# Kernel tuning notes

Hardware: AMD Instinct MI355X
Metric: run time of the kernel (lower is better)

## Reference

```python
import jax, jax.numpy as jnp
import numpy as np

HID = 5120
H_DEV = 16          # 128 heads / 8 devices
NOPE = 128
ROPE = 64
VDIM = 128
QH = NOPE + ROPE    # 192
Q_LORA = 1536
KV_LORA = 512
EPS = 1e-6
SCALE_DEV = 1.0 / 8.0
ROPE_BASE = 10000.0


def rmsnorm(x, w):
    var = jnp.mean(x * x, axis=-1, keepdims=True)
    return x * jax.lax.rsqrt(var + EPS) * w


def apply_rope(x, pos):
    # DeepSeek-V2: interleaved->blocked reorder, then rotate-half RoPE.
    d = x.shape[-1]
    x = jnp.concatenate([x[..., 0::2], x[..., 1::2]], axis=-1)
    inv = 1.0 / (ROPE_BASE ** (jnp.arange(0, d, 2, dtype=jnp.float32) / d))  # [d/2]
    ang = pos[:, None, :, None].astype(jnp.float32) * inv                     # [b,1,s,d/2]
    cos = jnp.concatenate([jnp.cos(ang), jnp.cos(ang)], axis=-1)
    sin = jnp.concatenate([jnp.sin(ang), jnp.sin(ang)], axis=-1)
    x1, x2 = x[..., : d // 2], x[..., d // 2:]
    return x * cos + jnp.concatenate([-x2, x1], axis=-1) * sin


def setup_inputs() -> dict:
    key = jax.random.key(0)
    ks = jax.random.split(key, 16)
    b, s, past = 1, 2048, 2048
    w = lambda k, shape: (jax.random.normal(k, shape, jnp.float32) * 0.02)
    return {
        "hidden_states": jax.random.normal(ks[0], (b, s, HID), jnp.float32),
        "position_ids": jnp.arange(b * s, dtype=jnp.int32).reshape(b, s),
        "attention_mask": jnp.zeros((b, 1, s, past + s), jnp.float32),
        "past_k": jax.random.normal(ks[1], (b, H_DEV, past, QH), jnp.float32),
        "past_v": jax.random.normal(ks[2], (b, H_DEV, past, VDIM), jnp.float32),
        "w_in_ln": jnp.ones((HID,), jnp.float32),
        "w_qa": w(ks[3], (Q_LORA, HID)),
        "w_qa_ln": jnp.ones((Q_LORA,), jnp.float32),
        "w_qb": w(ks[4], (H_DEV * QH, Q_LORA)),
        "w_kva": w(ks[5], (KV_LORA + ROPE, HID)),
        "w_kva_ln": jnp.ones((KV_LORA,), jnp.float32),
        "w_kvb": w(ks[6], (H_DEV * (NOPE + VDIM), KV_LORA)),
        "w_o": w(ks[7], (HID, H_DEV * VDIM)),
    }


def reference(hidden_states, position_ids, attention_mask, past_k, past_v,
              w_in_ln, w_qa, w_qa_ln, w_qb, w_kva, w_kva_ln, w_kvb, w_o):
    b, s, _ = hidden_states.shape
    residual = hidden_states * SCALE_DEV
    x = rmsnorm(hidden_states, w_in_ln)

    # MLA query: low-rank down, RMSNorm, up to per-device heads
    q = rmsnorm(x @ w_qa.T, w_qa_ln) @ w_qb.T                       # [b,s,H*QH]
    q = q.reshape(b, s, H_DEV, QH).transpose(0, 2, 1, 3)            # [b,H,s,QH]
    q_nope, q_pe = q[..., :NOPE], q[..., NOPE:]

    # MLA key/value: joint compressed kv + shared rope key
    ckv = x @ w_kva.T                                                # [b,s,KV_LORA+ROPE]
    c_kv, k_pe = ckv[..., :KV_LORA], ckv[..., KV_LORA:]
    kv = rmsnorm(c_kv, w_kva_ln) @ w_kvb.T                           # [b,s,H*(NOPE+V)]
    kv = kv.reshape(b, s, H_DEV, NOPE + VDIM).transpose(0, 2, 1, 3)  # [b,H,s,NOPE+V]
    k_nope, v = kv[..., :NOPE], kv[..., NOPE:]
    k_pe = k_pe.reshape(b, 1, s, ROPE)

    q_pe = apply_rope(q_pe, position_ids)
    k_pe = apply_rope(k_pe, position_ids)

    q = jnp.concatenate([q_nope, q_pe], axis=-1)                     # [b,H,s,QH]
    k = jnp.concatenate([k_nope, jnp.broadcast_to(k_pe, (b, H_DEV, s, ROPE))], axis=-1)

    # KV-cache concat -> present kv
    k = jnp.concatenate([past_k, k], axis=2)                         # [b,H,s_kv,QH]
    v = jnp.concatenate([past_v, v], axis=2)                         # [b,H,s_kv,V]

    scores = jnp.einsum('bhqd,bhkd->bhqk', q, k) * (QH ** -0.5) + attention_mask
    attn = jax.nn.softmax(scores, axis=-1)
    ctx = jnp.einsum('bhqk,bhkd->bhqd', attn, v)                     # [b,H,s,V]
    ctx = ctx.transpose(0, 2, 1, 3).reshape(b, s, H_DEV * VDIM)

    out = residual + ctx @ w_o.T
    return out.astype(jnp.float32), k.astype(jnp.float32), v.astype(jnp.float32)
```

## Files before the change

### kernel.cpp

```cpp
#include <hip/hip_runtime.h>
#include <cstdint>

typedef unsigned short ushort_t;
typedef __attribute__((ext_vector_type(8))) short short8;
typedef __attribute__((ext_vector_type(4))) float floatx4;

#define HID    5120
#define NHEAD  16
#define NOPE   128
#define ROPE_D 64
#define VDIM   128
#define QHD    192
#define QLORA  1536
#define KVLORA 512
#define SEQ    2048
#define PAST   2048
#define TOTK   4096
#define EPS_RMS 1e-6f
#define SCALE_DEV 0.125f
#define LOG2E 1.4426950408889634f
#define ATT_SCALE 0.07216878364870322f
#define LOG2_10000 13.287712379549449f

__device__ __forceinline__ float bf2f(ushort_t u) {
  unsigned int x = ((unsigned int)u) << 16;
  return __builtin_bit_cast(float, x);
}
__device__ __forceinline__ ushort_t f2bf(float f) {
  unsigned int u = __builtin_bit_cast(unsigned int, f);
  unsigned int r = u + 0x7fffu + ((u >> 16) & 1u);
  return (ushort_t)(r >> 16);
}
__device__ __forceinline__ void unpack8(uint4 c, float* f) {
  const ushort_t* p = (const ushort_t*)&c;
#pragma unroll
  for (int i = 0; i < 8; ++i) f[i] = bf2f(p[i]);
}
__device__ __forceinline__ uint4 pack8(const float* f) {
  uint4 c;
  ushort_t* p = (ushort_t*)&c;
#pragma unroll
  for (int i = 0; i < 8; ++i) p[i] = f2bf(f[i]);
  return c;
}

__global__ void cvt_kernel(const float* __restrict__ src, ushort_t* __restrict__ dst)
{
  long i = ((long)blockIdx.x * 256 + threadIdx.x) * 8;
  float f[8];
  *(float4*)(f)     = *(const float4*)(src + i);
  *(float4*)(f + 4) = *(const float4*)(src + i + 4);
  *(uint4*)(dst + i) = pack8(f);
}

#define GLDT 40
__global__ __launch_bounds__(256, 2) void gemm_bt(
    const ushort_t* __restrict__ A, const ushort_t* __restrict__ B,
    ushort_t* __restrict__ Cb, float* __restrict__ Cf,
    const float* __restrict__ resid, float resid_scale,
    int M, int N, int K)
{
  __shared__ __align__(16) ushort_t As[128 * GLDT];
  __shared__ __align__(16) ushort_t Bs[128 * GLDT];
  int t = threadIdx.x;
  int lane = t & 63, wave = t >> 6;
  int wm = wave >> 1, wn = wave & 1;
  int lrow = lane & 15, quad = lane >> 4;
  long bm = (long)blockIdx.y * 128;
  long bn = (long)blockIdx.x * 128;

  int r0 = t >> 2, cc = t & 3;
  int r1 = r0 + 64;
  const ushort_t* a0 = A + (bm + r0) * (long)K + cc * 8;
  const ushort_t* a1 = A + (bm + r1) * (long)K + cc * 8;
  long nb0 = bn + r0; if (nb0 > N - 1) nb0 = N - 1;
  long nb1 = bn + r1; if (nb1 > N - 1) nb1 = N - 1;
  const ushort_t* b0 = B + nb0 * (long)K + cc * 8;
  const ushort_t* b1 = B + nb1 * (long)K + cc * 8;

  floatx4 acc[4][4];
#pragma unroll
  for (int i = 0; i < 4; ++i)
#pragma unroll
    for (int j = 0; j < 4; ++j) acc[i][j] = (floatx4)0.f;

  uint4 pa0 = *(const uint4*)a0;
  uint4 pa1 = *(const uint4*)a1;
  uint4 pb0 = *(const uint4*)b0;
  uint4 pb1 = *(const uint4*)b1;

  int nk = K >> 5;
  for (int kt = 0; kt < nk; ++kt) {
    *(uint4*)&As[r0 * GLDT + cc * 8] = pa0;
    *(uint4*)&As[r1 * GLDT + cc * 8] = pa1;
    *(uint4*)&Bs[r0 * GLDT + cc * 8] = pb0;
    *(uint4*)&Bs[r1 * GLDT + cc * 8] = pb1;
    __syncthreads();
    if (kt + 1 < nk) {
      int off = (kt + 1) << 5;
      pa0 = *(const uint4*)(a0 + off);
      pa1 = *(const uint4*)(a1 + off);
      pb0 = *(const uint4*)(b0 + off);
      pb1 = *(const uint4*)(b1 + off);
    }
    short8 af[4], bfr[4];
#pragma unroll
    for (int mt = 0; mt < 4; ++mt)
      af[mt] = *(const short8*)&As[(wm * 64 + mt * 16 + lrow) * GLDT + quad * 8];
#pragma unroll
    for (int nt = 0; nt < 4; ++nt)
      bfr[nt] = *(const short8*)&Bs[(wn * 64 + nt * 16 + lrow) * GLDT + quad * 8];
#pragma unroll
    for (int mt = 0; mt < 4; ++mt)
#pragma unroll
      for (int nt = 0; nt < 4; ++nt)
        acc[mt][nt] = __builtin_amdgcn_mfma_f32_16x16x32_bf16(af[mt], bfr[nt], acc[mt][nt], 0, 0, 0);
    __syncthreads();
  }

#pragma unroll
  for (int mt = 0; mt < 4; ++mt) {
    long grow = bm + wm * 64 + mt * 16 + quad * 4;
#pragma unroll
    for (int nt = 0; nt < 4; ++nt) {
      long gcol = bn + wn * 64 + nt * 16 + lrow;
      if (gcol < N) {
#pragma unroll
        for (int r2 = 0; r2 < 4; ++r2) {
          long row = grow + r2;
          float v = acc[mt][nt][r2];
          if (Cf) {
            if (resid) v += resid_scale * resid[row * (long)N + gcol];
            Cf[row * (long)N + gcol] = v;
          } else {
            Cb[row * (long)N + gcol] = f2bf(v);
          }
        }
      }
    }
  }
}

__global__ void rms_in_kernel(const float* __restrict__ x,
                              const float* __restrict__ w,
                              ushort_t* __restrict__ out)
{
  int row = blockIdx.x, t = threadIdx.x;
  const float* xr = x + (long)row * HID + t * 16;
  float v[16];
#pragma unroll
  for (int i = 0; i < 4; ++i) *(float4*)(v + i * 4) = *(const float4*)(xr + i * 4);
  float ss = 0.f;
#pragma unroll
  for (int i = 0; i < 16; ++i) ss += v[i] * v[i];
#pragma unroll
  for (int o = 1; o < 64; o <<= 1) ss += __shfl_xor(ss, o);
  __shared__ float red[5];
  if ((t & 63) == 0) red[t >> 6] = ss;
  __syncthreads();
  float tot = red[0] + red[1] + red[2] + red[3] + red[4];
  float sc = rsqrtf(tot / (float)HID + EPS_RMS);
  float wv[16];
#pragma unroll
  for (int i = 0; i < 4; ++i) *(float4*)(wv + i * 4) = *(const float4*)(w + t * 16 + i * 4);
#pragma unroll
  for (int i = 0; i < 16; ++i) v[i] *= sc * wv[i];
  ushort_t* o = out + (long)row * HID + t * 16;
  *(uint4*)o       = pack8(v);
  *(uint4*)(o + 8) = pack8(v + 8);
}

__global__ void rms_qa_kernel(const ushort_t* __restrict__ x,
                              const float* __restrict__ w,
                              ushort_t* __restrict__ out)
{
  int row = blockIdx.x, t = threadIdx.x;
  const ushort_t* xr = x + (long)row * QLORA;
  float v[8];
  unpack8(*(const uint4*)(xr + t * 8), v);
  float ss = 0.f;
#pragma unroll
  for (int i = 0; i < 8; ++i) ss += v[i] * v[i];
#pragma unroll
  for (int o = 1; o < 64; o <<= 1) ss += __shfl_xor(ss, o);
  __shared__ float red[3];
  if ((t & 63) == 0) red[t >> 6] = ss;
  __syncthreads();
  float tot = red[0] + red[1] + red[2];
  float sc = rsqrtf(tot / (float)QLORA + EPS_RMS);
  float wv[8];
  *(float4*)(wv)     = *(const float4*)(w + t * 8);
  *(float4*)(wv + 4) = *(const float4*)(w + t * 8 + 4);
#pragma unroll
  for (int i = 0; i < 8; ++i) v[i] *= sc * wv[i];
  *(uint4*)(out + (long)row * QLORA + t * 8) = pack8(v);
}

__global__ void rms_ckv_rope(const ushort_t* __restrict__ ckv_raw,
                             const float* __restrict__ w,
                             const int* __restrict__ pos_ids,
                             ushort_t* __restrict__ ckv_n,
                             ushort_t* __restrict__ kpe,
                             float* __restrict__ k_out)
{
  int row = blockIdx.x, t = threadIdx.x;
  const ushort_t* xr = ckv_raw + (long)row * 576;
  float v[8];
  unpack8(*(const uint4*)(xr + t * 8), v);
  float ss = 0.f;
#pragma unroll
  for (int i = 0; i < 8; ++i) ss += v[i] * v[i];
#pragma unroll
  for (int o = 1; o < 64; o <<= 1) ss += __shfl_xor(ss, o);
  float sc = rsqrtf(ss / (float)KVLORA + EPS_RMS);
  float wv[8];
  *(float4*)(wv)     = *(const float4*)(w + t * 8);
  *(float4*)(wv + 4) = *(const float4*)(w + t * 8 + 4);
  float ov[8];
#pragma unroll
  for (int i = 0; i < 8; ++i) ov[i] = v[i] * sc * wv[i];
  *(uint4*)(ckv_n + (long)row * KVLORA + t * 8) = pack8(ov);

  if (t < 32) {
    float e  = bf2f(xr[512 + 2 * t]);
    float od = bf2f(xr[512 + 2 * t + 1]);
    float p = (float)pos_ids[row];
    float inv = __builtin_exp2f(-((float)t / 32.f) * LOG2_10000);
    float ang = p * inv, sn, cs;
    sincosf(ang, &sn, &cs);
    float r1 = e * cs - od * sn;
    float r2 = od * cs + e * sn;
    kpe[(long)row * 64 + t]      = f2bf(r1);
    kpe[(long)row * 64 + 32 + t] = f2bf(r2);
#pragma unroll
    for (int h = 0; h < NHEAD; ++h) {
      float* kr = k_out + ((long)h * TOTK + PAST + row) * QHD + NOPE;
      kr[t] = r1;
      kr[32 + t] = r2;
    }
  }
}

__global__ void qpost_kernel(const ushort_t* __restrict__ q_raw,
                             const int* __restrict__ pos_ids,
                             ushort_t* __restrict__ q_bf)
{
  int row = blockIdx.x, t = threadIdx.x;
  const ushort_t* qr = q_raw + (long)row * 3072;
  ushort_t* qo = q_bf + (long)row * 3072;
  {
    int hh = t >> 4, c = t & 15;
    float v[8];
    unpack8(*(const uint4*)(qr + hh * QHD + c * 8), v);
#pragma unroll
    for (int i = 0; i < 8; ++i) v[i] *= ATT_SCALE;
    *(uint4*)(qo + hh * QHD + c * 8) = pack8(v);
  }
  float p = (float)pos_ids[row];
#pragma unroll
  for (int it = 0; it < 2; ++it) {
    int slot = t + it * 256;
    int hh = slot >> 5, i = slot & 31;
    float e  = bf2f(qr[hh * QHD + NOPE + 2 * i]);
    float od = bf2f(qr[hh * QHD + NOPE + 2 * i + 1]);
    float inv = __builtin_exp2f(-((float)i / 32.f) * LOG2_10000);
    float ang = p * inv, sn, cs;
    sincosf(ang, &sn, &cs);
    qo[hh * QHD + NOPE + i]      = f2bf((e * cs - od * sn) * ATT_SCALE);
    qo[hh * QHD + NOPE + 32 + i] = f2bf((od * cs + e * sn) * ATT_SCALE);
  }
}

__global__ void kvpost_kernel(const ushort_t* __restrict__ kv_raw,
                              float* __restrict__ k_out,
                              float* __restrict__ v_out)
{
  int row = blockIdx.x, t = threadIdx.x;
  const ushort_t* kr = kv_raw + (long)row * 4096;
#pragma unroll
  for (int it = 0; it < 2; ++it) {
    int c = t + it * 256;
    int hh = c >> 5, cc = c & 31;
    float v[8];
    unpack8(*(const uint4*)(kr + c * 8), v);
    float* dst;
    if (cc < 16) dst = k_out + ((long)hh * TOTK + PAST + row) * QHD + cc * 8;
    else         dst = v_out + ((long)hh * TOTK + PAST + row) * VDIM + (cc - 16) * 8;
    floatx4 f0 = {v[0], v[1], v[2], v[3]};
    floatx4 f1 = {v[4], v[5], v[6], v[7]};
    *(floatx4*)dst = f0;
    *(floatx4*)(dst + 4) = f1;
  }
}

__global__ void past_kernel(const float* __restrict__ past_k,
                            const float* __restrict__ past_v,
                            float* __restrict__ k_out,
                            float* __restrict__ v_out)
{
  long c = (long)blockIdx.x * 256 + threadIdx.x;
  if (c < 1572864) {
    float4 v = *(const float4*)(past_k + c * 4);
    long hh = c / 98304, rem = c % 98304;
    long s = rem / 48, cc = rem % 48;
    *(float4*)(k_out + (hh * (long)TOTK + s) * QHD + cc * 4) = v;
  } else {
    long c2 = c - 1572864;
    float4 v = *(const float4*)(past_v + c2 * 4);
    long hh = c2 / 65536, rem = c2 % 65536;
    long s = rem / 32, cc = rem % 32;
    *(float4*)(v_out + (hh * (long)TOTK + s) * VDIM + cc * 4) = v;
  }
}

__global__ void buildK_kernel(const float* __restrict__ past_k,
                              const ushort_t* __restrict__ kv_raw,
                              const ushort_t* __restrict__ kpe,
                              ushort_t* __restrict__ Kc)
{
  long g = (long)blockIdx.x * 256 + threadIdx.x;
  int ko = (int)(g & 63);
  long r = g >> 6;
  int cc = (int)(r % 24);
  long r2 = r / 24;
  int kt = (int)(r2 & 63);
  int hh = (int)(r2 >> 6);
  int key = kt * 64 + ko;
  uint4 val;
  if (key < PAST) {
    const float* src = past_k + ((long)hh * PAST + key) * QHD + cc * 8;
    float f[8];
    *(float4*)(f)     = *(const float4*)src;
    *(float4*)(f + 4) = *(const float4*)(src + 4);
    val = pack8(f);
  } else {
    int s = key - PAST;
    int d0 = cc * 8;
    if (d0 < NOPE) val = *(const uint4*)(kv_raw + (long)s * 4096 + hh * 256 + d0);
    else           val = *(const uint4*)(kpe + (long)s * 64 + (d0 - NOPE));
  }
  *(uint4*)(Kc + g * 8) = val;
}

__global__ void buildV_kernel(const float* __restrict__ past_v,
                              const ushort_t* __restrict__ kv_raw,
                              ushort_t* __restrict__ Vc)
{
  long tid = (long)blockIdx.x * 256 + threadIdx.x;
  int vd = (int)(tid & 127);
  long r = tid >> 7;
  int kchunk = (int)(r & 7);
  long r2 = r >> 3;
  int kt = (int)(r2 & 63);
  int hh = (int)(r2 >> 6);
  int key0 = kt * 64 + kchunk * 8;
  __align__(16) ushort_t tmp[8];
  if (key0 < PAST) {
#pragma unroll
    for (int j = 0; j < 8; ++j)
      tmp[j] = f2bf(past_v[((long)hh * PAST + key0 + j) * VDIM + vd]);
  } else {
    int s = key0 - PAST;
#pragma unroll
    for (int j = 0; j < 8; ++j)
      tmp[j] = kv_raw[(long)(s + j) * 4096 + hh * 256 + NOPE + vd];
  }
  *(uint4*)(Vc + ((((long)hh * 64 + kt) * 128 + vd) * 9 + kchunk) * 8) = *(uint4*)tmp;
}

__global__ __launch_bounds__(256, 3) void attn_kernel(
    const ushort_t* __restrict__ qb,
    const ushort_t* __restrict__ Kc,
    const ushort_t* __restrict__ Vc,
    const float* __restrict__ attn_mask,
    ushort_t* __restrict__ opart,
    float* __restrict__ ml)
{
  __shared__ __align__(16) ushort_t KtL[1536 * 8];
  __shared__ __align__(16) ushort_t VtL[1152 * 8];
  __shared__ __align__(16) ushort_t Pl[4 * 16 * 72];

  int t = threadIdx.x, lane = t & 63, wave = t >> 6;
  int lrow = lane & 15, quad = lane >> 4;
  int lb = blockIdx.x;
  int xcd = lb & 7, j = lb >> 3;
  int h = xcd + 8 * (j / 96);
  int rem = j % 96;
  int sec = rem >> 5;
  int q0 = (rem & 31) * 64;
  int kt_beg = (sec == 0) ? 0 : (sec == 1 ? 22 : 43);
  int kt_end = (sec == 0) ? 22 : (sec == 1 ? 43 : 64);
  int qrow_a = q0 + wave * 16 + lrow;
  int qrow_c = q0 + wave * 16 + quad * 4;

  short8 aq[6];
  const ushort_t* qp = qb + ((long)qrow_a * 16 + h) * QHD + quad * 8;
#pragma unroll
  for (int kc = 0; kc < 6; ++kc) aq[kc] = *(const short8*)(qp + kc * 32);

  float m_r[4], l_r[4];
  floatx4 cacc[8];
#pragma unroll
  for (int r = 0; r < 4; ++r) { m_r[r] = -1e30f; l_r[r] = 0.f; }
#pragma unroll
  for (int v = 0; v < 8; ++v) cacc[v] = (floatx4)0.f;

  const ushort_t* Kbase = Kc + (long)h * 64 * 1536 * 8;
  const ushort_t* Vbase = Vc + (long)h * 64 * 1152 * 8;

  for (int kt2 = kt_beg; kt2 < kt_end; ++kt2) {
    const ushort_t* ks = Kbase + (long)kt2 * 1536 * 8;
#pragma unroll
    for (int i = 0; i < 6; ++i) {
      int s = i * 256 + t;
      *(uint4*)&KtL[s * 8] = *(const uint4*)(ks + (long)s * 8);
    }
    const ushort_t* vs = Vbase + (long)kt2 * 1152 * 8;
#pragma unroll
    for (int i = 0; i < 5; ++i) {
      int s = i * 256 + t;
      if (s < 1152) *(uint4*)&VtL[s * 8] = *(const uint4*)(vs + (long)s * 8);
    }
    __syncthreads();

    floatx4 sacc[4];
#pragma unroll
    for (int nt = 0; nt < 4; ++nt) sacc[nt] = (floatx4)0.f;
    __builtin_amdgcn_s_setprio(1);
#pragma unroll
    for (int kc = 0; kc < 6; ++kc) {
#pragma unroll
      for (int nt = 0; nt < 4; ++nt) {
        short8 bk = *(const short8*)&KtL[(((kc * 4 + quad) * 64) + nt * 16 + lrow) * 8];
        sacc[nt] = __builtin_amdgcn_mfma_f32_16x16x32_bf16(aq[kc], bk, sacc[nt], 0, 0, 0);
      }
    }
    __builtin_amdgcn_s_setprio(0);

    int kbase = kt2 * 64;
    float sv[4][4];
#pragma unroll
    for (int nt = 0; nt < 4; ++nt)
#pragma unroll
      for (int r = 0; r < 4; ++r)
        sv[nt][r] = sacc[nt][r] +
                    attn_mask[(long)(qrow_c + r) * TOTK + kbase + nt * 16 + lrow];

    float alpha[4];
#pragma unroll
    for (int r = 0; r < 4; ++r) {
      float mx = fmaxf(fmaxf(sv[0][r], sv[1][r]), fmaxf(sv[2][r], sv[3][r]));
      mx = fmaxf(mx, __shfl_xor(mx, 1));
      mx = fmaxf(mx, __shfl_xor(mx, 2));
      mx = fmaxf(mx, __shfl_xor(mx, 4));
      mx = fmaxf(mx, __shfl_xor(mx, 8));
      float mn = fmaxf(m_r[r], mx);
      alpha[r] = __builtin_exp2f((m_r[r] - mn) * LOG2E);
      m_r[r] = mn;
      float rs = 0.f;
#pragma unroll
      for (int nt = 0; nt < 4; ++nt) {
        float p = __builtin_exp2f((sv[nt][r] - mn) * LOG2E);
        sv[nt][r] = p;
        rs += p;
      }
      rs += __shfl_xor(rs, 1);
      rs += __shfl_xor(rs, 2);
      rs += __shfl_xor(rs, 4);
      rs += __shfl_xor(rs, 8);
      l_r[r] = l_r[r] * alpha[r] + rs;
    }
#pragma unroll
    for (int v = 0; v < 8; ++v) {
      floatx4 c = cacc[v];
      c[0] *= alpha[0]; c[1] *= alpha[1]; c[2] *= alpha[2]; c[3] *= alpha[3];
      cacc[v] = c;
    }

    ushort_t* pw = &Pl[wave * 16 * 72];
#pragma unroll
    for (int nt = 0; nt < 4; ++nt)
#pragma unroll
      for (int r = 0; r < 4; ++r)
        pw[(quad * 4 + r) * 72 + nt * 16 + lrow] = f2bf(sv[nt][r]);

    const ushort_t* pr = &Pl[wave * 16 * 72];
    short8 ap[2];
#pragma unroll
    for (int kc = 0; kc < 2; ++kc)
      ap[kc] = *(const short8*)(pr + lrow * 72 + kc * 32 + quad * 8);
    __builtin_amdgcn_s_setprio(1);
#pragma unroll
    for (int kc = 0; kc < 2; ++kc) {
#pragma unroll
      for (int v = 0; v < 8; ++v) {
        short8 bv = *(const short8*)&VtL[(((v * 16 + lrow) * 9) + kc * 4 + quad) * 8];
        cacc[v] = __builtin_amdgcn_mfma_f32_16x16x32_bf16(ap[kc], bv, cacc[v], 0, 0, 0);
      }
    }
    __builtin_amdgcn_s_setprio(0);
    __syncthreads();
  }

  long obase = (long)(sec * 16 + h) * 2048 + qrow_c;
#pragma unroll
  for (int v = 0; v < 8; ++v)
#pragma unroll
    for (int r = 0; r < 4; ++r)
      opart[(obase + r) * 128 + v * 16 + lrow] = f2bf(cacc[v][r]);
  if (lrow == 0) {
#pragma unroll
    for (int r = 0; r < 4; ++r) {
      float* mp = ml + (obase + r) * 2;
      mp[0] = m_r[r];
      mp[1] = l_r[r];
    }
  }
}

__global__ void combine_kernel(const ushort_t* __restrict__ opart,
                               const float* __restrict__ ml,
                               ushort_t* __restrict__ ctx)
{
  int t = threadIdx.x;
  int gr = blockIdx.x * 16 + (t >> 4);
  int h = gr >> 11, qrow = gr & 2047;
  int dc = (t & 15) * 8;
  float m[3], l[3];
#pragma unroll
  for (int s = 0; s < 3; ++s) {
    const float* p = ml + ((long)(s * 16 + h) * 2048 + qrow) * 2;
    m[s] = p[0]; l[s] = p[1];
  }
  float M = fmaxf(fmaxf(m[0], m[1]), m[2]);
  float aa[3], L = 0.f;
#pragma unroll
  for (int s = 0; s < 3; ++s) {
    aa[s] = __builtin_exp2f((m[s] - M) * LOG2E);
    L += aa[s] * l[s];
  }
  float inv = 1.f / L;
  float acc[8] = {0.f, 0.f, 0.f, 0.f, 0.f, 0.f, 0.f, 0.f};
#pragma unroll
  for (int s = 0; s < 3; ++s) {
    uint4 c = *(const uint4*)(opart + ((long)(s * 16 + h) * 2048 + qrow) * 128 + dc);
    float f[8];
    unpack8(c, f);
#pragma unroll
    for (int i = 0; i < 8; ++i) acc[i] += aa[s] * f[i];
  }
  float outv[8];
#pragma unroll
  for (int i = 0; i < 8; ++i) outv[i] = acc[i] * inv;
  *(uint4*)(ctx + (long)qrow * 2048 + h * 128 + dc) = pack8(outv);
}

extern "C" void kernel_launch(void* const* d_in, const int* in_sizes, int n_in,
                              void* d_out, int out_size, void* d_ws, size_t ws_size,
                              hipStream_t stream)
{
  const float* hidden   = (const float*)d_in[0];
  const int*   pos      = (const int*)d_in[1];
  const float* mask     = (const float*)d_in[2];
  const float* past_k   = (const float*)d_in[3];
  const float* past_v   = (const float*)d_in[4];
  const float* w_in_ln  = (const float*)d_in[5];
  const float* w_qa     = (const float*)d_in[6];
  const float* w_qa_ln  = (const float*)d_in[7];
  const float* w_qb     = (const float*)d_in[8];
  const float* w_kva    = (const float*)d_in[9];
  const float* w_kva_ln = (const float*)d_in[10];
  const float* w_kvb    = (const float*)d_in[11];
  const float* w_o      = (const float*)d_in[12];

  float* out0  = (float*)d_out;
  float* k_out = out0 + 10485760;
  float* v_out = k_out + 12582912;

  char* ws = (char*)d_ws;
  ushort_t* x_bf   = (ushort_t*)(ws + 0);
  ushort_t* q_raw  = x_bf;
  ushort_t* kv_raw = x_bf;
  ushort_t* qa_raw = (ushort_t*)(ws + 20971520);
  ushort_t* qa_n   = (ushort_t*)(ws + 27262976);
  ushort_t* ckv_raw= (ushort_t*)(ws + 33554432);
  ushort_t* ckv_n  = (ushort_t*)(ws + 35913728);
  ushort_t* kpe    = (ushort_t*)(ws + 38010880);
  ushort_t* q_bf   = (ushort_t*)(ws + 38273024);
  ushort_t* Kc     = (ushort_t*)(ws + 50855936);
  ushort_t* Vc     = (ushort_t*)(ws + 76021760);
  ushort_t* ctx    = (ushort_t*)(ws + 94896128);

  ushort_t* opart  = (ushort_t*)(ws + 0);
  float*    mlbuf  = (float*)(ws + 25165824);

  ushort_t* wqa_bf  = Kc;
  ushort_t* wkva_bf = (ushort_t*)(ws + 50855936 + 15728640);
  ushort_t* wqb_bf  = Vc;
  ushort_t* wkvb_bf = (ushort_t*)(ws + 76021760 + 9437184);
  ushort_t* wo_bf   = Kc;

  cvt_kernel<<<dim3(3840), dim3(256), 0, stream>>>(w_qa, wqa_bf);
  cvt_kernel<<<dim3(1440), dim3(256), 0, stream>>>(w_kva, wkva_bf);
  cvt_kernel<<<dim3(2304), dim3(256), 0, stream>>>(w_qb, wqb_bf);
  cvt_kernel<<<dim3(1024), dim3(256), 0, stream>>>(w_kvb, wkvb_bf);

  rms_in_kernel<<<dim3(2048), dim3(320), 0, stream>>>(hidden, w_in_ln, x_bf);

  gemm_bt<<<dim3(12, 16), dim3(256), 0, stream>>>(x_bf, wqa_bf, qa_raw, (float*)nullptr,
                                                  (const float*)nullptr, 0.f, 2048, 1536, 5120);
  gemm_bt<<<dim3(5, 16), dim3(256), 0, stream>>>(x_bf, wkva_bf, ckv_raw, (float*)nullptr,
                                                 (const float*)nullptr, 0.f, 2048, 576, 5120);

  rms_qa_kernel<<<dim3(2048), dim3(192), 0, stream>>>(qa_raw, w_qa_ln, qa_n);
  rms_ckv_rope<<<dim3(2048), dim3(64), 0, stream>>>(ckv_raw, w_kva_ln, pos, ckv_n, kpe, k_out);

  gemm_bt<<<dim3(24, 16), dim3(256), 0, stream>>>(qa_n, wqb_bf, q_raw, (float*)nullptr,
                                                  (const float*)nullptr, 0.f, 2048, 3072, 1536);
  qpost_kernel<<<dim3(2048), dim3(256), 0, stream>>>(q_raw, pos, q_bf);

  gemm_bt<<<dim3(32, 16), dim3(256), 0, stream>>>(ckv_n, wkvb_bf, kv_raw, (float*)nullptr,
                                                  (const float*)nullptr, 0.f, 2048, 4096, 512);
  kvpost_kernel<<<dim3(2048), dim3(256), 0, stream>>>(kv_raw, k_out, v_out);
  past_kernel<<<dim3(10240), dim3(256), 0, stream>>>(past_k, past_v, k_out, v_out);

  buildK_kernel<<<dim3(6144), dim3(256), 0, stream>>>(past_k, kv_raw, kpe, Kc);
  buildV_kernel<<<dim3(4096), dim3(256), 0, stream>>>(past_v, kv_raw, Vc);

  attn_kernel<<<dim3(1536), dim3(256), 0, stream>>>(q_bf, Kc, Vc, mask, opart, mlbuf);
  combine_kernel<<<dim3(2048), dim3(256), 0, stream>>>(opart, mlbuf, ctx);

  cvt_kernel<<<dim3(5120), dim3(256), 0, stream>>>(w_o, wo_bf);

  gemm_bt<<<dim3(40, 16), dim3(256), 0, stream>>>(ctx, wo_bf, (ushort_t*)nullptr, out0,
                                                  hidden, SCALE_DEV, 2048, 5120, 2048);
}
```

Before: 898.3 us.

## Fuse q_a and kv_a projections into one split-K GEMM and defer softmax rescale

Concatenates the w_qa and w_kva bf16 weights so both down-projections run as a single GEMM with N=2112, split along K into two halves that accumulate into a zeroed fp32 buffer with atomics. The RMSNorm/RoPE kernels now read fp32 directly from that buffer. The intent is to fill the GPU better than the two small separate GEMMs did (12x16 and 5x16 blocks) and to drop the bf16 rounding of intermediates. The cost is an extra zeroing pass and atomic traffic. Separately, the attention kernel skips the running-max update and the output accumulator rescale unless some row's max grows by more than 8. This is a lazy rescaling scheme that stays exact because l and the output share the same stale max.

```diff
diff --git a/kernel.cpp b/kernel.cpp
--- a/kernel.cpp
+++ b/kernel.cpp
@@ -16,6 +16,7 @@
 #define SEQ    2048
 #define PAST   2048
 #define TOTK   4096
+#define NQAKV  2112
 #define EPS_RMS 1e-6f
 #define SCALE_DEV 0.125f
 #define LOG2E 1.4426950408889634f
@@ -51,6 +52,13 @@
   *(float4*)(f)     = *(const float4*)(src + i);
   *(float4*)(f + 4) = *(const float4*)(src + i + 4);
   *(uint4*)(dst + i) = pack8(f);
+}
+
+__global__ void zero4_kernel(uint4* __restrict__ dst)
+{
+  long i = (long)blockIdx.x * 256 + threadIdx.x;
+  uint4 z; z.x = 0u; z.y = 0u; z.z = 0u; z.w = 0u;
+  dst[i] = z;
 }
 
 #define GLDT 40
@@ -141,6 +149,85 @@
   }
 }
 
+__global__ __launch_bounds__(256, 2) void gemm_splitk(
+    const ushort_t* __restrict__ A, const ushort_t* __restrict__ B,
+    float* __restrict__ Cf, int M, int N, int K)
+{
+  __shared__ __align__(16) ushort_t As[128 * GLDT];
+  __shared__ __align__(16) ushort_t Bs[128 * GLDT];
+  int t = threadIdx.x;
+  int lane = t & 63, wave = t >> 6;
+  int wm = wave >> 1, wn = wave & 1;
+  int lrow = lane & 15, quad = lane >> 4;
+  long bm = (long)blockIdx.y * 128;
+  long bn = (long)blockIdx.x * 128;
+  int khalf = K >> 1;
+  long k0 = (long)blockIdx.z * khalf;
+
+  int r0 = t >> 2, cc = t & 3;
+  int r1 = r0 + 64;
+  const ushort_t* a0 = A + (bm + r0) * (long)K + k0 + cc * 8;
+  const ushort_t* a1 = A + (bm + r1) * (long)K + k0 + cc * 8;
+  long nb0 = bn + r0; if (nb0 > N - 1) nb0 = N - 1;
+  long nb1 = bn + r1; if (nb1 > N - 1) nb1 = N - 1;
+  const ushort_t* b0 = B + nb0 * (long)K + k0 + cc * 8;
+  const ushort_t* b1 = B + nb1 * (long)K + k0 + cc * 8;
+
+  floatx4 acc[4][4];
+#pragma unroll
+  for (int i = 0; i < 4; ++i)
+#pragma unroll
+    for (int j = 0; j < 4; ++j) acc[i][j] = (floatx4)0.f;
+
+  uint4 pa0 = *(const uint4*)a0;
+  uint4 pa1 = *(const uint4*)a1;
+  uint4 pb0 = *(const uint4*)b0;
+  uint4 pb1 = *(const uint4*)b1;
+
+  int nk = khalf >> 5;
+  for (int kt = 0; kt < nk; ++kt) {
+    *(uint4*)&As[r0 * GLDT + cc * 8] = pa0;
+    *(uint4*)&As[r1 * GLDT + cc * 8] = pa1;
+    *(uint4*)&Bs[r0 * GLDT + cc * 8] = pb0;
+    *(uint4*)&Bs[r1 * GLDT + cc * 8] = pb1;
+    __syncthreads();
+    if (kt + 1 < nk) {
+      int off = (kt + 1) << 5;
+      pa0 = *(const uint4*)(a0 + off);
+      pa1 = *(const uint4*)(a1 + off);
+      pb0 = *(const uint4*)(b0 + off);
+      pb1 = *(const uint4*)(b1 + off);
+    }
+    short8 af[4], bfr[4];
+#pragma unroll
+    for (int mt = 0; mt < 4; ++mt)
+      af[mt] = *(const short8*)&As[(wm * 64 + mt * 16 + lrow) * GLDT + quad * 8];
+#pragma unroll
+    for (int nt = 0; nt < 4; ++nt)
+      bfr[nt] = *(const short8*)&Bs[(wn * 64 + nt * 16 + lrow) * GLDT + quad * 8];
+#pragma unroll
+    for (int mt = 0; mt < 4; ++mt)
+#pragma unroll
+      for (int nt = 0; nt < 4; ++nt)
+        acc[mt][nt] = __builtin_amdgcn_mfma_f32_16x16x32_bf16(af[mt], bfr[nt], acc[mt][nt], 0, 0, 0);
+    __syncthreads();
+  }
+
+#pragma unroll
+  for (int mt = 0; mt < 4; ++mt) {
+    long grow = bm + wm * 64 + mt * 16 + quad * 4;
+#pragma unroll
+    for (int nt = 0; nt < 4; ++nt) {
+      long gcol = bn + wn * 64 + nt * 16 + lrow;
+      if (gcol < N) {
+#pragma unroll
+        for (int r2 = 0; r2 < 4; ++r2)
+          atomicAdd(&Cf[(grow + r2) * (long)N + gcol], acc[mt][nt][r2]);
+      }
+    }
+  }
+}
+
 __global__ void rms_in_kernel(const float* __restrict__ x,
                               const float* __restrict__ w,
                               ushort_t* __restrict__ out)
@@ -170,14 +257,15 @@
   *(uint4*)(o + 8) = pack8(v + 8);
 }
 
-__global__ void rms_qa_kernel(const ushort_t* __restrict__ x,
-                              const float* __restrict__ w,
-                              ushort_t* __restrict__ out)
+__global__ void rms_qa_f32(const float* __restrict__ C,
+                           const float* __restrict__ w,
+                           ushort_t* __restrict__ out)
 {
   int row = blockIdx.x, t = threadIdx.x;
-  const ushort_t* xr = x + (long)row * QLORA;
+  const float* xr = C + (long)row * NQAKV + t * 8;
   float v[8];
-  unpack8(*(const uint4*)(xr + t * 8), v);
+  *(float4*)(v)     = *(const float4*)(xr);
+  *(float4*)(v + 4) = *(const float4*)(xr + 4);
   float ss = 0.f;
 #pragma unroll
   for (int i = 0; i < 8; ++i) ss += v[i] * v[i];
@@ -196,17 +284,18 @@
   *(uint4*)(out + (long)row * QLORA + t * 8) = pack8(v);
 }
 
-__global__ void rms_ckv_rope(const ushort_t* __restrict__ ckv_raw,
-                             const float* __restrict__ w,
-                             const int* __restrict__ pos_ids,
-                             ushort_t* __restrict__ ckv_n,
-                             ushort_t* __restrict__ kpe,
-                             float* __restrict__ k_out)
+__global__ void rms_ckv_rope_f32(const float* __restrict__ C,
+                                 const float* __restrict__ w,
+                                 const int* __restrict__ pos_ids,
+                                 ushort_t* __restrict__ ckv_n,
+                                 ushort_t* __restrict__ kpe,
+                                 float* __restrict__ k_out)
 {
   int row = blockIdx.x, t = threadIdx.x;
-  const ushort_t* xr = ckv_raw + (long)row * 576;
+  const float* xr = C + (long)row * NQAKV + QLORA;
   float v[8];
-  unpack8(*(const uint4*)(xr + t * 8), v);
+  *(float4*)(v)     = *(const float4*)(xr + t * 8);
+  *(float4*)(v + 4) = *(const float4*)(xr + t * 8 + 4);
   float ss = 0.f;
 #pragma unroll
   for (int i = 0; i < 8; ++i) ss += v[i] * v[i];
@@ -222,8 +311,8 @@
   *(uint4*)(ckv_n + (long)row * KVLORA + t * 8) = pack8(ov);
 
   if (t < 32) {
-    float e  = bf2f(xr[512 + 2 * t]);
-    float od = bf2f(xr[512 + 2 * t + 1]);
+    float e  = xr[512 + 2 * t];
+    float od = xr[512 + 2 * t + 1];
     float p = (float)pos_ids[row];
     float inv = __builtin_exp2f(-((float)t / 32.f) * LOG2_10000);
     float ang = p * inv, sn, cs;
@@ -446,7 +535,7 @@
         sv[nt][r] = sacc[nt][r] +
                     attn_mask[(long)(qrow_c + r) * TOTK + kbase + nt * 16 + lrow];
 
-    float alpha[4];
+    float mxv[4]; int need = 0;
 #pragma unroll
     for (int r = 0; r < 4; ++r) {
       float mx = fmaxf(fmaxf(sv[0][r], sv[1][r]), fmaxf(sv[2][r], sv[3][r]));
@@ -454,13 +543,30 @@
       mx = fmaxf(mx, __shfl_xor(mx, 2));
       mx = fmaxf(mx, __shfl_xor(mx, 4));
       mx = fmaxf(mx, __shfl_xor(mx, 8));
-      float mn = fmaxf(m_r[r], mx);
-      alpha[r] = __builtin_exp2f((m_r[r] - mn) * LOG2E);
-      m_r[r] = mn;
+      mxv[r] = mx;
+      need |= (mx > m_r[r] + 8.f) ? 1 : 0;
+    }
+    float alpha[4] = {1.f, 1.f, 1.f, 1.f};
+    if (__any(need)) {
+#pragma unroll
+      for (int r = 0; r < 4; ++r) {
+        float mn = fmaxf(m_r[r], mxv[r]);
+        alpha[r] = __builtin_exp2f((m_r[r] - mn) * LOG2E);
+        m_r[r] = mn;
+      }
+#pragma unroll
+      for (int v = 0; v < 8; ++v) {
+        floatx4 c = cacc[v];
+        c[0] *= alpha[0]; c[1] *= alpha[1]; c[2] *= alpha[2]; c[3] *= alpha[3];
+        cacc[v] = c;
+      }
+    }
+#pragma unroll
+    for (int r = 0; r < 4; ++r) {
       float rs = 0.f;
 #pragma unroll
       for (int nt = 0; nt < 4; ++nt) {
-        float p = __builtin_exp2f((sv[nt][r] - mn) * LOG2E);
+        float p = __builtin_exp2f((sv[nt][r] - m_r[r]) * LOG2E);
         sv[nt][r] = p;
         rs += p;
       }
@@ -469,12 +575,6 @@
       rs += __shfl_xor(rs, 4);
       rs += __shfl_xor(rs, 8);
       l_r[r] = l_r[r] * alpha[r] + rs;
-    }
-#pragma unroll
-    for (int v = 0; v < 8; ++v) {
-      floatx4 c = cacc[v];
-      c[0] *= alpha[0]; c[1] *= alpha[1]; c[2] *= alpha[2]; c[3] *= alpha[3];
-      cacc[v] = c;
     }
 
     ushort_t* pw = &Pl[wave * 16 * 72];
@@ -581,39 +681,38 @@
   ushort_t* x_bf   = (ushort_t*)(ws + 0);
   ushort_t* q_raw  = x_bf;
   ushort_t* kv_raw = x_bf;
-  ushort_t* qa_raw = (ushort_t*)(ws + 20971520);
-  ushort_t* qa_n   = (ushort_t*)(ws + 27262976);
-  ushort_t* ckv_raw= (ushort_t*)(ws + 33554432);
-  ushort_t* ckv_n  = (ushort_t*)(ws + 35913728);
-  ushort_t* kpe    = (ushort_t*)(ws + 38010880);
+  float*    Cqakv  = (float*)(ws + 20971520);
+  ushort_t* qa_n   = (ushort_t*)(ws + 38273024);
   ushort_t* q_bf   = (ushort_t*)(ws + 38273024);
   ushort_t* Kc     = (ushort_t*)(ws + 50855936);
   ushort_t* Vc     = (ushort_t*)(ws + 76021760);
+  ushort_t* ckv_n  = (ushort_t*)(ws + 94896128);
+  ushort_t* kpe    = (ushort_t*)(ws + 96993280);
   ushort_t* ctx    = (ushort_t*)(ws + 94896128);
 
   ushort_t* opart  = (ushort_t*)(ws + 0);
   float*    mlbuf  = (float*)(ws + 25165824);
 
-  ushort_t* wqa_bf  = Kc;
-  ushort_t* wkva_bf = (ushort_t*)(ws + 50855936 + 15728640);
-  ushort_t* wqb_bf  = Vc;
-  ushort_t* wkvb_bf = (ushort_t*)(ws + 76021760 + 9437184);
-  ushort_t* wo_bf   = Kc;
-
-  cvt_kernel<<<dim3(3840), dim3(256), 0, stream>>>(w_qa, wqa_bf);
-  cvt_kernel<<<dim3(1440), dim3(256), 0, stream>>>(w_kva, wkva_bf);
+  ushort_t* wqakva_bf = Kc;
+  ushort_t* wqb_bf    = Vc;
+  ushort_t* wkvb_bf   = (ushort_t*)(ws + 76021760 + 9437184);
+  ushort_t* wo_bf     = Kc;
+
+  cvt_kernel<<<dim3(3840), dim3(256), 0, stream>>>(w_qa, wqakva_bf);
+  cvt_kernel<<<dim3(1440), dim3(256), 0, stream>>>(w_kva, wqakva_bf + 7864320);
   cvt_kernel<<<dim3(2304), dim3(256), 0, stream>>>(w_qb, wqb_bf);
   cvt_kernel<<<dim3(1024), dim3(256), 0, stream>>>(w_kvb, wkvb_bf);
 
+  zero4_kernel<<<dim3(4224), dim3(256), 0, stream>>>((uint4*)Cqakv);
+
   rms_in_kernel<<<dim3(2048), dim3(320), 0, stream>>>(hidden, w_in_ln, x_bf);
 
-  gemm_bt<<<dim3(12, 16), dim3(256), 0, stream>>>(x_bf, wqa_bf, qa_raw, (float*)nullptr,
-                                                  (const float*)nullptr, 0.f, 2048, 1536, 5120);
-  gemm_bt<<<dim3(5, 16), dim3(256), 0, stream>>>(x_bf, wkva_bf, ckv_raw, (float*)nullptr,
-                                                 (const float*)nullptr, 0.f, 2048, 576, 5120);
-
-  rms_qa_kernel<<<dim3(2048), dim3(192), 0, stream>>>(qa_raw, w_qa_ln, qa_n);
-  rms_ckv_rope<<<dim3(2048), dim3(64), 0, stream>>>(ckv_raw, w_kva_ln, pos, ckv_n, kpe, k_out);
+  gemm_splitk<<<dim3(17, 16, 2), dim3(256), 0, stream>>>(x_bf, wqakva_bf, Cqakv,
+                                                         2048, NQAKV, 5120);
+
+  rms_qa_f32<<<dim3(2048), dim3(192), 0, stream>>>(Cqakv, w_qa_ln, qa_n);
+  rms_ckv_rope_f32<<<dim3(2048), dim3(64), 0, stream>>>(Cqakv, w_kva_ln, pos,
+                                                        ckv_n, kpe, k_out);
 
   gemm_bt<<<dim3(24, 16), dim3(256), 0, stream>>>(qa_n, wqb_bf, q_raw, (float*)nullptr,
                                                   (const float*)nullptr, 0.f, 2048, 3072, 1536);
```

Measured after the change: 813.2 us. 1.1x faster.
